# Optimization experiments

Measured on AMD Instinct MI355X. Metric: run time of the kernel, lower is better.

The kernel has to match this reference:

```python
import jax, jax.numpy as jnp
import numpy as np

# ---- config (matches init_kwargs) ----
VOCAB = 50000
D_MODEL = 256
N_HEADS = 8
N_LAYERS = 2
N_KERNELS = 11
D_FF = 2048  # torch TransformerEncoderLayer default
D_HEAD = D_MODEL // N_HEADS
LN_EPS = 1e-5


def kernel_mus(n):
    mus = [1.0]
    bin_size = 2.0 / (n - 1)
    mus.append(1 - bin_size / 2)
    for i in range(1, n - 1):
        mus.append(mus[i] - bin_size)
    return mus


def kernel_sigmas(n):
    bin_size = 2.0 / (n - 1)
    return [0.0001] + [0.5 * bin_size] * (n - 1)

MU = jnp.asarray(kernel_mus(N_KERNELS), dtype=jnp.float32)      # [K]
SIGMA = jnp.asarray(kernel_sigmas(N_KERNELS), dtype=jnp.float32)  # [K]


def pos_encoding(seq_len, d):
    pos = jnp.arange(seq_len, dtype=jnp.float32)[:, None]
    div = jnp.exp(jnp.arange(0, d, 2, dtype=jnp.float32) * (-np.log(10000.0) / d))
    pe = jnp.zeros((seq_len, d), dtype=jnp.float32)
    pe = pe.at[:, 0::2].set(jnp.sin(pos * div)).at[:, 1::2].set(jnp.cos(pos * div))
    return pe


def layer_norm(x, scale, bias):
    m = jnp.mean(x, axis=-1, keepdims=True)
    v = jnp.mean(jnp.square(x - m), axis=-1, keepdims=True)
    return (x - m) * jax.lax.rsqrt(v + LN_EPS) * scale + bias


def encoder(x, Wqkv, bqkv, Wo, bo, ln1_s, ln1_b, W1, b1, W2, b2, ln2_s, ln2_b):
    # x: [B,S,d]; params stacked over layers on axis 0. Post-LN, ReLU (torch defaults).
    B, S, d = x.shape

    def layer(x, p):
        wqkv, bq, wo, bob, l1s, l1b, w1, b1_, w2, b2_, l2s, l2b = p
        qkv = jnp.einsum('bsd,ed->bse', x, wqkv) + bq          # [B,S,3d]
        q, k, v = jnp.split(qkv, 3, axis=-1)
        def split_heads(t):
            return t.reshape(B, S, N_HEADS, D_HEAD).transpose(0, 2, 1, 3)
        q, k, v = split_heads(q), split_heads(k), split_heads(v)
        scores = jnp.einsum('bhqe,bhke->bhqk', q, k) / np.sqrt(D_HEAD)
        attn = jax.nn.softmax(scores, axis=-1)
        o = jnp.einsum('bhqk,bhke->bhqe', attn, v).transpose(0, 2, 1, 3).reshape(B, S, d)
        o = jnp.einsum('bsd,ed->bse', o, wo) + bob
        x = layer_norm(x + o, l1s, l1b)
        h = jax.nn.relu(jnp.einsum('bsd,fd->bsf', x, w1) + b1_)
        h = jnp.einsum('bsf,df->bsd', h, w2) + b2_
        x = layer_norm(x + h, l2s, l2b)
        return x, None

    x, _ = jax.lax.scan(layer, x, (Wqkv, bqkv, Wo, bo, ln1_s, ln1_b, W1, b1, W2, b2, ln2_s, ln2_b))
    return x


def setup_inputs() -> dict:
    key = jax.random.key(0)
    ks = jax.random.split(key, 16)
    B, Q, D = 256, 32, 256
    inp = {
        'query_ids': jax.random.randint(ks[0], (B, Q), 1, VOCAB),   # >0 so mask is all-ones
        'doc_ids': jax.random.randint(ks[1], (B, D), 1, VOCAB),
        'emb': jax.random.normal(ks[2], (VOCAB, D_MODEL), jnp.float32) * 0.1,
        'a': jnp.full((1, 1, 1), 0.5, jnp.float32),
        'mlp_w': jax.random.normal(ks[3], (1, N_KERNELS), jnp.float32) * 0.1,
        'Wqkv': jax.random.normal(ks[4], (N_LAYERS, 3 * D_MODEL, D_MODEL), jnp.float32) * 0.05,
        'bqkv': jnp.zeros((N_LAYERS, 3 * D_MODEL), jnp.float32),
        'Wo': jax.random.normal(ks[5], (N_LAYERS, D_MODEL, D_MODEL), jnp.float32) * 0.05,
        'bo': jnp.zeros((N_LAYERS, D_MODEL), jnp.float32),
        'ln1_s': jnp.ones((N_LAYERS, D_MODEL), jnp.float32),
        'ln1_b': jnp.zeros((N_LAYERS, D_MODEL), jnp.float32),
        'W1': jax.random.normal(ks[6], (N_LAYERS, D_FF, D_MODEL), jnp.float32) * 0.03,
        'b1': jnp.zeros((N_LAYERS, D_FF), jnp.float32),
        'W2': jax.random.normal(ks[7], (N_LAYERS, D_MODEL, D_FF), jnp.float32) * 0.03,
        'b2': jnp.zeros((N_LAYERS, D_MODEL), jnp.float32),
        'ln2_s': jnp.ones((N_LAYERS, D_MODEL), jnp.float32),
        'ln2_b': jnp.zeros((N_LAYERS, D_MODEL), jnp.float32),
    }
    return inp


def reference(query_ids, doc_ids, emb, a, mlp_w, Wqkv, bqkv, Wo, bo,
              ln1_s, ln1_b, W1, b1, W2, b2, ln2_s, ln2_b):
    enc_p = (Wqkv, bqkv, Wo, bo, ln1_s, ln1_b, W1, b1, W2, b2, ln2_s, ln2_b)
    q_mask = (query_ids > 0).astype(jnp.float32)   # [B,Q]
    d_mask = (doc_ids > 0).astype(jnp.float32)     # [B,D]
    q_emb = emb[query_ids] * q_mask[..., None]     # [B,Q,d]
    d_emb = emb[doc_ids] * d_mask[..., None]       # [B,D,d]
    q_ctx = encoder(2.0 * q_emb + pos_encoding(q_emb.shape[1], D_MODEL)[None], *enc_p)
    d_ctx = encoder(2.0 * d_emb + pos_encoding(d_emb.shape[1], D_MODEL)[None], *enc_p)
    q_mix = (a * q_emb + (1.0 - a) * q_ctx) * q_mask[..., None]
    d_mix = (a * d_emb + (1.0 - a) * d_ctx) * d_mask[..., None]
    sim = jnp.einsum('bqe,bke->bqk', q_mix, d_mix)                    # [B,Q,D]
    K = jnp.exp(-jnp.square(sim[..., None] - MU) / (2.0 * jnp.square(SIGMA)))  # [B,Q,D,K]
    K_masked = K * q_mask[:, :, None, None] * d_mask[:, None, :, None]
    query_kernel = jnp.sum(K_masked, axis=2)                          # [B,Q,K]
    log_qk = jnp.log(jnp.clip(query_kernel, 1e-10, None)) * q_mask[..., None]
    per_kernel = jnp.sum(log_qk, axis=1)                              # [B,K]
    score_log = (per_kernel @ mlp_w.T)[:, 0]
    len_norm = jnp.sum(query_kernel / K_masked.shape[2], axis=1)      # [B,K]
    score_len = (len_norm @ mlp_w.T)[:, 0]
    return score_log + score_len                                      # [B]
```

## Files before the change

kernel.cpp:

```cpp
#include <hip/hip_runtime.h>
#include <math.h>


#define DMODEL 256
typedef float f32x4 __attribute__((ext_vector_type(4)));

__global__ __launch_bounds__(256) void k_pe(float* __restrict__ pe) {
  int s = blockIdx.x, d = threadIdx.x;
  int i2 = d & ~1;
  float freq = expf((float)i2 * (-9.210340371976184f / 256.f));
  float ang = (float)s * freq;
  pe[s * 256 + d] = (d & 1) ? cosf(ang) : sinf(ang);
}

__global__ __launch_bounds__(256) void k_embed(const int* __restrict__ dids,
    const int* __restrict__ qids, const float* __restrict__ emb,
    const float* __restrict__ pe, float* __restrict__ out_x) {
  int tid = threadIdx.x;
  int tok = blockIdx.x * 4 + (tid >> 6);
  int lane = tid & 63;
  int d0 = lane * 4;
  int id, s;
  if (tok < 65536) { id = dids[tok]; s = tok & 255; }
  else             { id = qids[tok - 65536]; s = (tok - 65536) & 31; }
  float m = id > 0 ? 2.f : 0.f;
  float4 e = *(const float4*)(emb + (size_t)id * DMODEL + d0);
  float4 p = *(const float4*)(pe + s * 256 + d0);
  float4 o;
  o.x = m * e.x + p.x; o.y = m * e.y + p.y;
  o.z = m * e.z + p.z; o.w = m * e.w + p.w;
  *(float4*)(out_x + (size_t)tok * DMODEL + d0) = o;
}

template<bool RELU>
__global__ __launch_bounds__(256) void k_gemm(const float* __restrict__ X,
    const float* __restrict__ W, const float* __restrict__ bias,
    float* __restrict__ out, int M, int N, int K) {
  __shared__ float As[2][16][128];
  __shared__ float Bs[2][16][128];
  int n0 = blockIdx.x * 128;
  int m0 = blockIdx.y * 128;
  int tid = threadIdx.x;
  const int wv = tid >> 6, lane = tid & 63;
  const int r8 = lane >> 3, c8 = lane & 7;
  const int R0 = (wv & 1) * 64 + r8 * 4;
  const int C0 = (wv >> 1) * 64 + c8 * 4;
  int lr = tid >> 1;
  int lk = (tid & 1) << 3;
  const float* Xp = X + (size_t)(m0 + lr) * K + lk;
  const float* Wp = W + (size_t)(n0 + lr) * K + lk;

  float acc[8][8];
#pragma unroll
  for (int i = 0; i < 8; ++i)
#pragma unroll
    for (int j = 0; j < 8; ++j) acc[i][j] = 0.f;

  float4 a0, a1, b0, b1;

#define GLOADT(KT) do { \
    a0 = *(const float4*)(Xp + (KT)); a1 = *(const float4*)(Xp + (KT) + 4); \
    b0 = *(const float4*)(Wp + (KT)); b1 = *(const float4*)(Wp + (KT) + 4); } while (0)

#define LWRITE(BUF) do { \
    As[BUF][lk + 0][lr] = a0.x; As[BUF][lk + 1][lr] = a0.y; \
    As[BUF][lk + 2][lr] = a0.z; As[BUF][lk + 3][lr] = a0.w; \
    As[BUF][lk + 4][lr] = a1.x; As[BUF][lk + 5][lr] = a1.y; \
    As[BUF][lk + 6][lr] = a1.z; As[BUF][lk + 7][lr] = a1.w; \
    Bs[BUF][lk + 0][lr] = b0.x; Bs[BUF][lk + 1][lr] = b0.y; \
    Bs[BUF][lk + 2][lr] = b0.z; Bs[BUF][lk + 3][lr] = b0.w; \
    Bs[BUF][lk + 4][lr] = b1.x; Bs[BUF][lk + 5][lr] = b1.y; \
    Bs[BUF][lk + 6][lr] = b1.z; Bs[BUF][lk + 7][lr] = b1.w; } while (0)

#define COMPT(BUF) do { \
    _Pragma("unroll") \
    for (int k = 0; k < 16; ++k) { \
      float av[8], bv[8]; \
      *(float4*)&av[0] = *(const float4*)&As[BUF][k][R0]; \
      *(float4*)&av[4] = *(const float4*)&As[BUF][k][R0 + 32]; \
      *(float4*)&bv[0] = *(const float4*)&Bs[BUF][k][C0]; \
      *(float4*)&bv[4] = *(const float4*)&Bs[BUF][k][C0 + 32]; \
      _Pragma("unroll") \
      for (int i = 0; i < 8; ++i) \
        _Pragma("unroll") \
        for (int j = 0; j < 8; ++j) \
          acc[i][j] += av[i] * bv[j]; \
    } } while (0)

  const int nt = K >> 4;
  GLOADT(0);
  LWRITE(0);
  __syncthreads();
  for (int t = 0; t < nt; t += 2) {
    int k1 = (t + 1) * 16;
    GLOADT(k1);
    COMPT(0);
    LWRITE(1);
    __syncthreads();
    if (t + 2 < nt) {
      int k2 = (t + 2) * 16;
      GLOADT(k2);
      COMPT(1);
      LWRITE(0);
    } else {
      COMPT(1);
    }
    __syncthreads();
  }
#undef GLOADT
#undef LWRITE
#undef COMPT

#pragma unroll
  for (int i = 0; i < 8; ++i) {
    int mr = m0 + (wv & 1) * 64 + ((i < 4) ? (r8 * 4 + i) : (32 + r8 * 4 + i - 4));
#pragma unroll
    for (int jb = 0; jb < 2; ++jb) {
      int nc = n0 + (wv >> 1) * 64 + jb * 32 + c8 * 4;
      float4 bz = *(const float4*)(bias + nc);
      float4 o4;
      o4.x = acc[i][jb * 4 + 0] + bz.x;
      o4.y = acc[i][jb * 4 + 1] + bz.y;
      o4.z = acc[i][jb * 4 + 2] + bz.z;
      o4.w = acc[i][jb * 4 + 3] + bz.w;
      if (RELU) {
        o4.x = fmaxf(o4.x, 0.f); o4.y = fmaxf(o4.y, 0.f);
        o4.z = fmaxf(o4.z, 0.f); o4.w = fmaxf(o4.w, 0.f);
      }
      *(float4*)(out + (size_t)mr * N + nc) = o4;
    }
  }
}

__global__ __launch_bounds__(256) void k_gemm_ln(const float* __restrict__ X,
    const float* __restrict__ W, const float* __restrict__ bias,
    float* __restrict__ xres, const float* __restrict__ lns,
    const float* __restrict__ lnb, int M, int K) {
  __shared__ float As[2][16][64];
  __shared__ float Bs[2][16][256];
  const int tid = threadIdx.x;
  const int m0 = blockIdx.x * 64;
  const int tx = tid & 15, ty = tid >> 4;
  const int rowA = tid & 63;
  const int kqA = (tid >> 6) << 2;
  const float* Xp = X + (size_t)(m0 + rowA) * K + kqA;
  const float* Wp = W + (size_t)tid * K;

  f32x4 acc[4][4];
#pragma unroll
  for (int r = 0; r < 4; ++r)
#pragma unroll
    for (int q = 0; q < 4; ++q) acc[r][q] = 0.f;

  f32x4 a, b0, b1, b2, b3;

#define GL(KT) do { \
    a  = *(const f32x4*)(Xp + (KT)); \
    b0 = *(const f32x4*)(Wp + (KT));      b1 = *(const f32x4*)(Wp + (KT) + 4); \
    b2 = *(const f32x4*)(Wp + (KT) + 8);  b3 = *(const f32x4*)(Wp + (KT) + 12); } while (0)

#define LW(BUF) do { \
    As[BUF][kqA + 0][rowA] = a[0]; As[BUF][kqA + 1][rowA] = a[1]; \
    As[BUF][kqA + 2][rowA] = a[2]; As[BUF][kqA + 3][rowA] = a[3]; \
    Bs[BUF][ 0][tid] = b0[0]; Bs[BUF][ 1][tid] = b0[1]; \
    Bs[BUF][ 2][tid] = b0[2]; Bs[BUF][ 3][tid] = b0[3]; \
    Bs[BUF][ 4][tid] = b1[0]; Bs[BUF][ 5][tid] = b1[1]; \
    Bs[BUF][ 6][tid] = b1[2]; Bs[BUF][ 7][tid] = b1[3]; \
    Bs[BUF][ 8][tid] = b2[0]; Bs[BUF][ 9][tid] = b2[1]; \
    Bs[BUF][10][tid] = b2[2]; Bs[BUF][11][tid] = b2[3]; \
    Bs[BUF][12][tid] = b3[0]; Bs[BUF][13][tid] = b3[1]; \
    Bs[BUF][14][tid] = b3[2]; Bs[BUF][15][tid] = b3[3]; } while (0)

#define CP(BUF) do { \
    _Pragma("unroll") \
    for (int k = 0; k < 16; ++k) { \
      f32x4 av = *(const f32x4*)&As[BUF][k][ty * 4]; \
      f32x4 bv0 = *(const f32x4*)&Bs[BUF][k][tx * 4]; \
      f32x4 bv1 = *(const f32x4*)&Bs[BUF][k][64 + tx * 4]; \
      f32x4 bv2 = *(const f32x4*)&Bs[BUF][k][128 + tx * 4]; \
      f32x4 bv3 = *(const f32x4*)&Bs[BUF][k][192 + tx * 4]; \
      _Pragma("unroll") \
      for (int r = 0; r < 4; ++r) { \
        acc[r][0] += av[r] * bv0; acc[r][1] += av[r] * bv1; \
        acc[r][2] += av[r] * bv2; acc[r][3] += av[r] * bv3; \
      } \
    } } while (0)

  const int nt = K >> 4;
  GL(0);
  LW(0);
  __syncthreads();
  for (int t = 0; t < nt; t += 2) {
    GL((t + 1) * 16);
    CP(0);
    LW(1);
    __syncthreads();
    if (t + 2 < nt) {
      GL((t + 2) * 16);
      CP(1);
      LW(0);
    } else {
      CP(1);
    }
    __syncthreads();
  }
#undef GL
#undef LW
#undef CP

  f32x4 bza[4], sca[4], lba[4];
#pragma unroll
  for (int q = 0; q < 4; ++q) {
    int c = q * 64 + tx * 4;
    bza[q] = *(const f32x4*)(bias + c);
    sca[q] = *(const f32x4*)(lns + c);
    lba[q] = *(const f32x4*)(lnb + c);
  }
#pragma unroll
  for (int r = 0; r < 4; ++r) {
    size_t row = (size_t)m0 + ty * 4 + r;
    f32x4 v[4];
    float ps = 0.f;
#pragma unroll
    for (int q = 0; q < 4; ++q) {
      f32x4 xr = *(const f32x4*)(xres + row * 256 + q * 64 + tx * 4);
      v[q] = acc[r][q] + bza[q] + xr;
      ps += v[q][0] + v[q][1] + v[q][2] + v[q][3];
    }
    ps += __shfl_xor(ps, 1); ps += __shfl_xor(ps, 2);
    ps += __shfl_xor(ps, 4); ps += __shfl_xor(ps, 8);
    float mean = ps * (1.f / 256.f);
    float ss = 0.f;
#pragma unroll
    for (int q = 0; q < 4; ++q) {
      v[q] -= mean;
      ss += v[q][0] * v[q][0] + v[q][1] * v[q][1]
          + v[q][2] * v[q][2] + v[q][3] * v[q][3];
    }
    ss += __shfl_xor(ss, 1); ss += __shfl_xor(ss, 2);
    ss += __shfl_xor(ss, 4); ss += __shfl_xor(ss, 8);
    float rs = rsqrtf(ss * (1.f / 256.f) + 1e-5f);
#pragma unroll
    for (int q = 0; q < 4; ++q) {
      f32x4 y = v[q] * rs * sca[q] + lba[q];
      *(f32x4*)(xres + row * 256 + q * 64 + tx * 4) = y;
    }
  }
}

__global__ __launch_bounds__(256) void k_attn_doc(const float* __restrict__ qkv,
    float* __restrict__ o, int b0) {
  __shared__ f32x4 Ks[256 * 8];
  __shared__ f32x4 Vs[256 * 8];
  int bl = blockIdx.x >> 3, h = blockIdx.x & 7;
  int tid = threadIdx.x;
  const float* base = qkv + (size_t)bl * 256 * 768;
  int hc = h * 32;
  for (int idx = tid; idx < 2048; idx += 256) {
    int s = idx >> 3, w = idx & 7;
    Ks[idx] = *(const f32x4*)(base + (size_t)s * 768 + 256 + hc + w * 4);
    Vs[idx] = *(const f32x4*)(base + (size_t)s * 768 + 512 + hc + w * 4);
  }
  __syncthreads();
  f32x4 q[8], acc[8];
  const float* qp = base + (size_t)tid * 768 + hc;
#pragma unroll
  for (int w = 0; w < 8; ++w) { q[w] = *(const f32x4*)(qp + 4 * w); acc[w] = 0.f; }
  float m = -1e30f, l = 0.f;
  const float scale = 0.17677669529663687f;
  for (int j = 0; j < 256; ++j) {
    const f32x4* kr = &Ks[j * 8];
    f32x4 da = q[0] * kr[0];
    f32x4 db = q[1] * kr[1];
#pragma unroll
    for (int w = 2; w < 8; w += 2) {
      da += q[w] * kr[w];
      db += q[w + 1] * kr[w + 1];
    }
    f32x4 d4 = da + db;
    float s_ = (d4[0] + d4[1] + d4[2] + d4[3]) * scale;
    float mn = fmaxf(m, s_);
    float p = __expf(s_ - mn);
    if (mn > m) {
      float al = __expf(m - mn);
      l *= al;
#pragma unroll
      for (int w = 0; w < 8; ++w) acc[w] *= al;
      m = mn;
    }
    l += p;
    const f32x4* vr = &Vs[j * 8];
#pragma unroll
    for (int w = 0; w < 8; ++w) acc[w] += p * vr[w];
  }
  float inv = 1.f / l;
  float* op = o + ((size_t)(b0 + bl) * 256 + tid) * DMODEL + hc;
#pragma unroll
  for (int w = 0; w < 8; ++w) *(f32x4*)(op + 4 * w) = acc[w] * inv;
}

__global__ __launch_bounds__(256) void k_attn_qry(const float* __restrict__ qkv,
    float* __restrict__ o) {
  __shared__ f32x4 Ks[32 * 64];
  __shared__ f32x4 Vs[32 * 64];
  int bl = blockIdx.x;
  int tid = threadIdx.x;
  const float* base = qkv + (size_t)bl * 32 * 768;
  for (int idx = tid; idx < 2048; idx += 256) {
    int s = idx >> 6, c = idx & 63;
    Ks[idx] = *(const f32x4*)(base + (size_t)s * 768 + 256 + c * 4);
    Vs[idx] = *(const f32x4*)(base + (size_t)s * 768 + 512 + c * 4);
  }
  __syncthreads();
  int h = tid >> 5, row = tid & 31;
  int hc = h * 32;
  f32x4 q[8], acc[8];
  const float* qp = base + (size_t)row * 768 + hc;
#pragma unroll
  for (int w = 0; w < 8; ++w) { q[w] = *(const f32x4*)(qp + 4 * w); acc[w] = 0.f; }
  float m = -1e30f, l = 0.f;
  const float scale = 0.17677669529663687f;
  for (int j = 0; j < 32; ++j) {
    const f32x4* kr = &Ks[j * 64 + h * 8];
    f32x4 da = q[0] * kr[0];
    f32x4 db = q[1] * kr[1];
#pragma unroll
    for (int w = 2; w < 8; w += 2) {
      da += q[w] * kr[w];
      db += q[w + 1] * kr[w + 1];
    }
    f32x4 d4 = da + db;
    float s_ = (d4[0] + d4[1] + d4[2] + d4[3]) * scale;
    float mn = fmaxf(m, s_);
    float p = __expf(s_ - mn);
    if (mn > m) {
      float al = __expf(m - mn);
      l *= al;
#pragma unroll
      for (int w = 0; w < 8; ++w) acc[w] *= al;
      m = mn;
    }
    l += p;
    const f32x4* vr = &Vs[j * 64 + h * 8];
#pragma unroll
    for (int w = 0; w < 8; ++w) acc[w] += p * vr[w];
  }
  float inv = 1.f / l;
  float* op = o + ((size_t)bl * 32 + row) * DMODEL + hc;
#pragma unroll
  for (int w = 0; w < 8; ++w) *(f32x4*)(op + 4 * w) = acc[w] * inv;
}

__global__ __launch_bounds__(256) void k_score(
    const int* __restrict__ qids, const int* __restrict__ dids,
    const float* __restrict__ emb, const float* __restrict__ xq,
    const float* __restrict__ xd, const float* __restrict__ a_ptr,
    const float* __restrict__ mlp_w, float* __restrict__ out) {
  __shared__ float qmix[32 * 256];
  __shared__ float qks[32 * 11];
  __shared__ float qmask_s[32];
  int b = blockIdx.x, tid = threadIdx.x;
  float av = a_ptr[0], aw = 1.f - av;
  for (int q = 0; q < 32; ++q) {
    int qid = qids[b * 32 + q];
    float qm = qid > 0 ? 1.f : 0.f;
    float ev = emb[(size_t)qid * 256 + tid];
    float xv = xq[((size_t)b * 32 + q) * 256 + tid];
    qmix[q * 256 + tid] = (av * ev + aw * xv) * qm;
    if (tid == 0) qmask_s[q] = qm;
  }
  for (int i = tid; i < 352; i += 256) qks[i] = 0.f;
  __syncthreads();
  int j = tid;
  int did = dids[b * 256 + j];
  float dmask = did > 0 ? 1.f : 0.f;
  float sim[32];
#pragma unroll
  for (int q = 0; q < 32; ++q) sim[q] = 0.f;
  const float4* de = (const float4*)(emb + (size_t)did * 256);
  const float4* dxp = (const float4*)(xd + ((size_t)b * 256 + j) * 256);
  for (int c = 0; c < 4; ++c) {
    float4 dreg[16];
#pragma unroll
    for (int w = 0; w < 16; ++w) {
      float4 e = de[c * 16 + w], x = dxp[c * 16 + w];
      dreg[w].x = av * e.x + aw * x.x;
      dreg[w].y = av * e.y + aw * x.y;
      dreg[w].z = av * e.z + aw * x.z;
      dreg[w].w = av * e.w + aw * x.w;
    }
#pragma unroll
    for (int q = 0; q < 32; ++q) {
      const float4* qp = (const float4*)&qmix[q * 256 + c * 64];
      float d_ = 0.f;
#pragma unroll
      for (int w = 0; w < 16; ++w) {
        float4 t = qp[w];
        d_ += t.x * dreg[w].x + t.y * dreg[w].y + t.z * dreg[w].z + t.w * dreg[w].w;
      }
      sim[q] += d_;
    }
  }
  const float MU[11] = {1.f, 0.9f, 0.7f, 0.5f, 0.3f, 0.1f, -0.1f, -0.3f, -0.5f, -0.7f, -0.9f};
  const float IC[11] = {5e7f, 50.f, 50.f, 50.f, 50.f, 50.f, 50.f, 50.f, 50.f, 50.f, 50.f};
  for (int q = 0; q < 32; ++q) {
    float s = sim[q];
    float f = dmask * qmask_s[q];
#pragma unroll
    for (int k = 0; k < 11; ++k) {
      float d_ = s - MU[k];
      float v = expf(-d_ * d_ * IC[k]) * f;
#pragma unroll
      for (int o = 32; o > 0; o >>= 1) v += __shfl_xor(v, o);
      if ((tid & 63) == 0) atomicAdd(&qks[q * 11 + k], v);
    }
  }
  __syncthreads();
  if (tid < 32) {
    float qm = qmask_s[tid];
    float p = 0.f;
#pragma unroll
    for (int k = 0; k < 11; ++k) {
      float qv = qks[tid * 11 + k];
      p += mlp_w[k] * (qm * logf(fmaxf(qv, 1e-10f)) + qv * (1.f / 256.f));
    }
#pragma unroll
    for (int o = 16; o > 0; o >>= 1) p += __shfl_xor(p, o);
    if (tid == 0) out[b] = p;
  }
}

extern "C" void kernel_launch(void* const* d_in, const int* in_sizes, int n_in,
                              void* d_out, int out_size, void* d_ws, size_t ws_size,
                              hipStream_t stream) {
  const int* qids = (const int*)d_in[0];
  const int* dids = (const int*)d_in[1];
  const float* emb = (const float*)d_in[2];
  const float* a = (const float*)d_in[3];
  const float* mlp_w = (const float*)d_in[4];
  const float* Wqkv = (const float*)d_in[5];
  const float* bqkv = (const float*)d_in[6];
  const float* Wo = (const float*)d_in[7];
  const float* bo = (const float*)d_in[8];
  const float* l1s = (const float*)d_in[9];
  const float* l1b = (const float*)d_in[10];
  const float* W1 = (const float*)d_in[11];
  const float* b1 = (const float*)d_in[12];
  const float* W2 = (const float*)d_in[13];
  const float* b2 = (const float*)d_in[14];
  const float* l2s = (const float*)d_in[15];
  const float* l2b = (const float*)d_in[16];
  float* out = (float*)d_out;
  float* ws = (float*)d_ws;

  const int TOK = 73728;
  const size_t QRY_QKV = (size_t)8192 * 768;

  size_t wsf = ws_size / 4;
  const size_t fixed = 2 * (size_t)TOK * 256 + 65536;
  const int cbs[] = {256, 128, 64, 32, 16, 8};
  const int fcs[] = {24576, 12288, 9216, 6144, 3072, 2048};
  int CB = 8, FC = 2048;
  for (int i = 0; i < 6; ++i) {
    size_t sc = (size_t)cbs[i] * 196608;
    size_t s2 = (size_t)fcs[i] * 2048;
    size_t scr = sc > s2 ? sc : s2;
    if (scr < QRY_QKV) scr = QRY_QKV;
    if (fixed + scr <= wsf) { CB = cbs[i]; FC = fcs[i]; break; }
  }

  float* x       = ws;
  float* t0      = x + (size_t)TOK * 256;
  float* pe      = t0 + (size_t)TOK * 256;
  float* scratch = pe + 65536;

  k_pe<<<256, 256, 0, stream>>>(pe);
  k_embed<<<TOK / 4, 256, 0, stream>>>(dids, qids, emb, pe, x);

  for (int l = 0; l < 2; ++l) {
    const float* wq = Wqkv + (size_t)l * 768 * 256;
    const float* bq = bqkv + l * 768;
    const float* wo = Wo + (size_t)l * 256 * 256;
    const float* bo_ = bo + l * 256;
    const float* w1 = W1 + (size_t)l * 2048 * 256;
    const float* b1_ = b1 + l * 2048;
    const float* w2 = W2 + (size_t)l * 256 * 2048;
    const float* b2_ = b2 + l * 256;

    for (int c = 0; c < 256; c += CB) {
      int Mc = CB * 256;
      k_gemm<false><<<dim3(6, Mc / 128), 256, 0, stream>>>(
          x + (size_t)c * 65536, wq, bq, scratch, Mc, 768, 256);
      k_attn_doc<<<CB * 8, 256, 0, stream>>>(scratch, t0, c);
    }
    k_gemm<false><<<dim3(6, 64), 256, 0, stream>>>(
        x + (size_t)65536 * 256, wq, bq, scratch, 8192, 768, 256);
    k_attn_qry<<<256, 256, 0, stream>>>(scratch, t0 + (size_t)65536 * 256);
    k_gemm_ln<<<TOK / 64, 256, 0, stream>>>(t0, wo, bo_, x,
        l1s + l * 256, l1b + l * 256, TOK, 256);
    for (int f = 0; f < TOK; f += FC) {
      k_gemm<true><<<dim3(16, FC / 128), 256, 0, stream>>>(
          x + (size_t)f * 256, w1, b1_, scratch, FC, 2048, 256);
      k_gemm_ln<<<FC / 64, 256, 0, stream>>>(scratch, w2, b2_, x + (size_t)f * 256,
          l2s + l * 256, l2b + l * 256, FC, 2048);
    }
  }

  k_score<<<256, 256, 0, stream>>>(qids, dids, emb, x + (size_t)65536 * 256,
                                   x, a, mlp_w, out);
}
```

Measured before the change: 6.844 ms.

## Split FFN along hidden dimension with accumulating W2 GEMM and separate add+LayerNorm

The FFN is restructured to slice the 2048-wide hidden dimension into FW-wide slabs over all tokens, not chunking over tokens. Each slab runs a W1 GEMM followed by a W2 GEMM that accumulates into a full-size output buffer. A new add+LayerNorm kernel then finishes the residual. This replaces the fused gemm_ln with K=2048 with plain GEMMs of higher parallelism, at the cost of extra reads and writes of the output buffer per slab and an extra LN pass.

```diff
diff --git a/kernel.cpp b/kernel.cpp
--- a/kernel.cpp
+++ b/kernel.cpp
@@ -32,10 +32,10 @@
   *(float4*)(out_x + (size_t)tok * DMODEL + d0) = o;
 }
 
-template<bool RELU>
+template<bool RELU, bool ACC>
 __global__ __launch_bounds__(256) void k_gemm(const float* __restrict__ X,
     const float* __restrict__ W, const float* __restrict__ bias,
-    float* __restrict__ out, int M, int N, int K) {
+    float* __restrict__ out, int M, int N, int K, int ldw) {
   __shared__ float As[2][16][128];
   __shared__ float Bs[2][16][128];
   int n0 = blockIdx.x * 128;
@@ -48,7 +48,7 @@
   int lr = tid >> 1;
   int lk = (tid & 1) << 3;
   const float* Xp = X + (size_t)(m0 + lr) * K + lk;
-  const float* Wp = W + (size_t)(n0 + lr) * K + lk;
+  const float* Wp = W + (size_t)(n0 + lr) * ldw + lk;
 
   float acc[8][8];
 #pragma unroll
@@ -117,12 +117,20 @@
 #pragma unroll
     for (int jb = 0; jb < 2; ++jb) {
       int nc = n0 + (wv >> 1) * 64 + jb * 32 + c8 * 4;
-      float4 bz = *(const float4*)(bias + nc);
       float4 o4;
-      o4.x = acc[i][jb * 4 + 0] + bz.x;
-      o4.y = acc[i][jb * 4 + 1] + bz.y;
-      o4.z = acc[i][jb * 4 + 2] + bz.z;
-      o4.w = acc[i][jb * 4 + 3] + bz.w;
+      if (ACC) {
+        float4 pv = *(const float4*)(out + (size_t)mr * N + nc);
+        o4.x = acc[i][jb * 4 + 0] + pv.x;
+        o4.y = acc[i][jb * 4 + 1] + pv.y;
+        o4.z = acc[i][jb * 4 + 2] + pv.z;
+        o4.w = acc[i][jb * 4 + 3] + pv.w;
+      } else {
+        float4 bz = *(const float4*)(bias + nc);
+        o4.x = acc[i][jb * 4 + 0] + bz.x;
+        o4.y = acc[i][jb * 4 + 1] + bz.y;
+        o4.z = acc[i][jb * 4 + 2] + bz.z;
+        o4.w = acc[i][jb * 4 + 3] + bz.w;
+      }
       if (RELU) {
         o4.x = fmaxf(o4.x, 0.f); o4.y = fmaxf(o4.y, 0.f);
         o4.z = fmaxf(o4.z, 0.f); o4.w = fmaxf(o4.w, 0.f);
@@ -246,6 +254,35 @@
       *(f32x4*)(xres + row * 256 + q * 64 + tx * 4) = y;
     }
   }
+}
+
+__global__ __launch_bounds__(256) void k_addln(float* __restrict__ x,
+    const float* __restrict__ t, const float* __restrict__ sc,
+    const float* __restrict__ bi) {
+  int tid = threadIdx.x;
+  size_t tok = (size_t)blockIdx.x * 4 + (tid >> 6);
+  int lane = tid & 63;
+  float4 xv = *(const float4*)(x + tok * 256 + lane * 4);
+  float4 tv = *(const float4*)(t + tok * 256 + lane * 4);
+  float4 v;
+  v.x = xv.x + tv.x; v.y = xv.y + tv.y; v.z = xv.z + tv.z; v.w = xv.w + tv.w;
+  float s1 = v.x + v.y + v.z + v.w;
+#pragma unroll
+  for (int o = 32; o > 0; o >>= 1) s1 += __shfl_xor(s1, o);
+  float mean = s1 * (1.f / 256.f);
+  float dx = v.x - mean, dy = v.y - mean, dz = v.z - mean, dw = v.w - mean;
+  float s2 = dx * dx + dy * dy + dz * dz + dw * dw;
+#pragma unroll
+  for (int o = 32; o > 0; o >>= 1) s2 += __shfl_xor(s2, o);
+  float rs = rsqrtf(s2 * (1.f / 256.f) + 1e-5f);
+  float4 s4 = *(const float4*)(sc + lane * 4);
+  float4 b4 = *(const float4*)(bi + lane * 4);
+  float4 ov;
+  ov.x = dx * rs * s4.x + b4.x;
+  ov.y = dy * rs * s4.y + b4.y;
+  ov.z = dz * rs * s4.z + b4.z;
+  ov.w = dw * rs * s4.w + b4.w;
+  *(float4*)(x + tok * 256 + lane * 4) = ov;
 }
 
 __global__ __launch_bounds__(256) void k_attn_doc(const float* __restrict__ qkv,
@@ -458,16 +495,19 @@
 
   size_t wsf = ws_size / 4;
   const size_t fixed = 2 * (size_t)TOK * 256 + 65536;
-  const int cbs[] = {256, 128, 64, 32, 16, 8};
-  const int fcs[] = {24576, 12288, 9216, 6144, 3072, 2048};
-  int CB = 8, FC = 2048;
-  for (int i = 0; i < 6; ++i) {
-    size_t sc = (size_t)cbs[i] * 196608;
-    size_t s2 = (size_t)fcs[i] * 2048;
-    size_t scr = sc > s2 ? sc : s2;
-    if (scr < QRY_QKV) scr = QRY_QKV;
-    if (fixed + scr <= wsf) { CB = cbs[i]; FC = fcs[i]; break; }
-  }
+  const int fws[] = {512, 256, 128};
+  const int cbs[] = {128, 64, 32};
+  int FW = 128, CB = 32;
+  for (int i = 0; i < 3; ++i) {
+    size_t scr = (size_t)TOK * fws[i];
+    size_t sc2 = (size_t)cbs[i] * 196608;
+    if (sc2 > scr) scr = sc2;
+    if (QRY_QKV > scr) scr = QRY_QKV;
+    if (fixed + scr <= wsf) { FW = fws[i]; CB = cbs[i]; break; }
+  }
+  size_t scrN = (size_t)TOK * FW;
+  { size_t sc2 = (size_t)CB * 196608; if (sc2 > scrN) scrN = sc2;
+    if (QRY_QKV > scrN) scrN = QRY_QKV; }
 
   float* x       = ws;
   float* t0      = x + (size_t)TOK * 256;
@@ -489,21 +529,27 @@
 
     for (int c = 0; c < 256; c += CB) {
       int Mc = CB * 256;
-      k_gemm<false><<<dim3(6, Mc / 128), 256, 0, stream>>>(
-          x + (size_t)c * 65536, wq, bq, scratch, Mc, 768, 256);
+      k_gemm<false, false><<<dim3(6, Mc / 128), 256, 0, stream>>>(
+          x + (size_t)c * 65536, wq, bq, scratch, Mc, 768, 256, 256);
       k_attn_doc<<<CB * 8, 256, 0, stream>>>(scratch, t0, c);
     }
-    k_gemm<false><<<dim3(6, 64), 256, 0, stream>>>(
-        x + (size_t)65536 * 256, wq, bq, scratch, 8192, 768, 256);
+    k_gemm<false, false><<<dim3(6, 64), 256, 0, stream>>>(
+        x + (size_t)65536 * 256, wq, bq, scratch, 8192, 768, 256, 256);
     k_attn_qry<<<256, 256, 0, stream>>>(scratch, t0 + (size_t)65536 * 256);
     k_gemm_ln<<<TOK / 64, 256, 0, stream>>>(t0, wo, bo_, x,
         l1s + l * 256, l1b + l * 256, TOK, 256);
-    for (int f = 0; f < TOK; f += FC) {
-      k_gemm<true><<<dim3(16, FC / 128), 256, 0, stream>>>(
-          x + (size_t)f * 256, w1, b1_, scratch, FC, 2048, 256);
-      k_gemm_ln<<<FC / 64, 256, 0, stream>>>(scratch, w2, b2_, x + (size_t)f * 256,
-          l2s + l * 256, l2b + l * 256, FC, 2048);
-    }
+    int nparts = 2048 / FW;
+    for (int p = 0; p < nparts; ++p) {
+      k_gemm<true, false><<<dim3(FW / 128, TOK / 128), 256, 0, stream>>>(
+          x, w1 + (size_t)p * FW * 256, b1_ + p * FW, scratch, TOK, FW, 256, 256);
+      if (p == 0)
+        k_gemm<false, false><<<dim3(2, TOK / 128), 256, 0, stream>>>(
+            scratch, w2, b2_, t0, TOK, 256, FW, 2048);
+      else
+        k_gemm<false, true><<<dim3(2, TOK / 128), 256, 0, stream>>>(
+            scratch, w2 + (size_t)p * FW, b2_, t0, TOK, 256, FW, 2048);
+    }
+    k_addln<<<TOK / 4, 256, 0, stream>>>(x, t0, l2s + l * 256, l2b + l * 256);
   }
 
   k_score<<<256, 256, 0, stream>>>(qids, dids, emb, x + (size_t)65536 * 256,
```

Result: faster. 6.548 ms (-4.3%).
